# Optimization experiments

Measured on AMD Instinct MI355X. Metric: run time of the kernel, lower is better.

Reference implementation:

```python
import jax, jax.numpy as jnp
import numpy as np

EMBED_DIM = 256
NUM_HEADS = 8
HEAD_DIM = EMBED_DIM // NUM_HEADS
WINDOW = 31
B, S = 4, 2048


def _make_params(key):
    ks = jax.random.split(key, 8)
    sc = 0.05
    Wq = jax.random.normal(ks[0], (NUM_HEADS, EMBED_DIM, HEAD_DIM), jnp.float32) * sc
    bq = jax.random.normal(ks[1], (NUM_HEADS, HEAD_DIM), jnp.float32) * sc
    Wk = jax.random.normal(ks[2], (NUM_HEADS, EMBED_DIM, HEAD_DIM), jnp.float32) * sc
    bk = jax.random.normal(ks[3], (NUM_HEADS, HEAD_DIM), jnp.float32) * sc
    Wv = jax.random.normal(ks[4], (NUM_HEADS, EMBED_DIM, HEAD_DIM), jnp.float32) * sc
    bv = jax.random.normal(ks[5], (NUM_HEADS, HEAD_DIM), jnp.float32) * sc
    Wo = jax.random.normal(ks[6], (NUM_HEADS * HEAD_DIM, EMBED_DIM), jnp.float32) * sc
    bo = jax.random.normal(ks[7], (EMBED_DIM,), jnp.float32) * sc
    return Wq, bq, Wk, bk, Wv, bv, Wo, bo


def setup_inputs() -> dict:
    key = jax.random.key(0)
    k1, k2, k3, k4 = jax.random.split(key, 4)
    eeg = jax.random.normal(k1, (B, S, EMBED_DIM), jnp.float32)
    pps = jax.random.normal(k2, (B, S, EMBED_DIM), jnp.float32)
    e2p = _make_params(k3)
    p2e = _make_params(k4)
    names = ["Wq", "bq", "Wk", "bk", "Wv", "bv", "Wo", "bo"]
    inp = {"eeg": eeg, "pps": pps}
    for n, p in zip(names, e2p):
        inp["e2p_" + n] = p
    for n, p in zip(names, p2e):
        inp["p2e_" + n] = p
    return inp


def _cross_window_attn(q_seq, kv_seq, Wq, bq, Wk, bk, Wv, bv, Wo, bo, window):
    # q_seq, kv_seq: [B, S, D]. Each query position i attends to window of
    # the zero-padded kv sequence centered at i (pad positions get bias-only k/v,
    # matching torch Linear applied to zero vectors).
    b, s, d_in = q_seq.shape
    h, _, hd = Wq.shape
    pad = (window - 1) // 2
    kv_pad = jnp.pad(kv_seq, ((0, 0), (pad, pad), (0, 0)))
    Q = jnp.einsum('bsd,hde->bhse', q_seq, Wq) + bq[None, :, None, :]
    K = jnp.einsum('bsd,hde->bhse', kv_pad, Wk) + bk[None, :, None, :]
    V = jnp.einsum('bsd,hde->bhse', kv_pad, Wv) + bv[None, :, None, :]
    idx = jnp.arange(s)[:, None] + jnp.arange(window)[None, :]  # [S, W]
    Kw = K[:, :, idx, :]  # [B, H, S, W, hd]
    Vw = V[:, :, idx, :]
    scores = jnp.einsum('bhse,bhswe->bhsw', Q, Kw) / np.sqrt(hd).astype(np.float32)
    attn = jax.nn.softmax(scores, axis=-1)
    out = jnp.einsum('bhsw,bhswe->bhse', attn, Vw)  # [B, H, S, hd]
    out = out.transpose(0, 2, 1, 3).reshape(b, s, h * hd)
    return out @ Wo + bo


def reference(eeg, pps,
              e2p_Wq, e2p_bq, e2p_Wk, e2p_bk, e2p_Wv, e2p_bv, e2p_Wo, e2p_bo,
              p2e_Wq, p2e_bq, p2e_Wk, p2e_bk, p2e_Wv, p2e_bv, p2e_Wo, p2e_bo):
    fused_eeg = _cross_window_attn(eeg, pps, e2p_Wq, e2p_bq, e2p_Wk, e2p_bk,
                                   e2p_Wv, e2p_bv, e2p_Wo, e2p_bo, WINDOW)
    fused_pps = _cross_window_attn(pps, eeg, p2e_Wq, p2e_bq, p2e_Wk, p2e_bk,
                                   p2e_Wv, p2e_bv, p2e_Wo, p2e_bo, WINDOW)
    return fused_eeg, fused_pps
```

## Files before the change

kernel.cpp:

```cpp
#include <hip/hip_runtime.h>

static __device__ __forceinline__ float bf2f(unsigned short u) {
    return __uint_as_float(((unsigned int)u) << 16);
}
static __device__ __forceinline__ unsigned short f2bf(float f) {
    unsigned int x = __float_as_uint(f);
    unsigned int lsb = (x >> 16) & 1u;
    x += 0x7fffu + lsb;
    return (unsigned short)(x >> 16);
}

typedef __attribute__((ext_vector_type(8))) short short8;
typedef __attribute__((ext_vector_type(4))) float floatx4;

static __device__ __forceinline__ short8 ldg8(const unsigned short* p) {
    short8 v; __builtin_memcpy(&v, p, 16); return v;
}

__global__ __launch_bounds__(256) void repack_kernel(
    const float* e2p_Wq, const float* e2p_bq,
    const float* e2p_Wk, const float* e2p_bk,
    const float* e2p_Wv, const float* e2p_bv,
    const float* e2p_Wo, const float* e2p_bo,
    const float* p2e_Wq, const float* p2e_bq,
    const float* p2e_Wk, const float* p2e_bk,
    const float* p2e_Wv, const float* p2e_bv,
    const float* p2e_Wo, const float* p2e_bo,
    const float* eeg, const float* pps,
    unsigned short* Wpack, unsigned short* Wopack, float* bias_pack, float* bias2,
    unsigned short* Abf)
{
    int idx = blockIdx.x * 256 + threadIdx.x;
    const int WP = 2 * 768 * 256;
    if (idx < WP) {
        int inp = idx / (768 * 256);
        int rem = idx % (768 * 256);
        int n = rem / 256, k = rem % 256;
        int proj = n / 256, h = (n % 256) / 32, e = n % 32;
        const float* W;
        if (inp == 0) W = (proj == 0) ? e2p_Wq : (proj == 1) ? p2e_Wk : p2e_Wv;
        else          W = (proj == 0) ? p2e_Wq : (proj == 1) ? e2p_Wk : e2p_Wv;
        Wpack[idx] = f2bf(W[h * 8192 + k * 32 + e]);
    }
    int idx2 = idx - WP;
    if (idx2 >= 0 && idx2 < 2 * 65536) {
        int dir = idx2 / 65536, rem2 = idx2 % 65536;
        int n = rem2 / 256, k = rem2 % 256;
        Wopack[idx2] = f2bf((dir == 0 ? e2p_Wo : p2e_Wo)[k * 256 + n]);
    }
    if (idx < 1536) {
        int inp = idx / 768, n = idx % 768;
        int proj = n / 256, he = n % 256;
        const float* bsrc;
        if (inp == 0) bsrc = (proj == 0) ? e2p_bq : (proj == 1) ? p2e_bk : p2e_bv;
        else          bsrc = (proj == 0) ? p2e_bq : (proj == 1) ? e2p_bk : e2p_bv;
        bias_pack[idx] = bsrc[he];
    }
    if (idx >= 1536 && idx < 2048) {
        int j = idx - 1536;
        int dir = j / 256, n = j % 256;
        bias2[j] = (dir == 0 ? e2p_bo : p2e_bo)[n];
    }
    {
        long base = (long)idx * 8;
        const float* src = (base < 2097152) ? eeg : pps;
        long off = (base < 2097152) ? base : base - 2097152;
        float v[8];
        __builtin_memcpy(v, src + off, 32);
        unsigned short o[8];
        #pragma unroll
        for (int j = 0; j < 8; ++j) o[j] = f2bf(v[j]);
        __builtin_memcpy(Abf + base, o, 16);
    }
}

template<bool C_F32>
__global__ __launch_bounds__(256) void mfma_gemm_kernel(
    const unsigned short* __restrict__ A0, const unsigned short* __restrict__ A1,
    const unsigned short* __restrict__ B0t, const unsigned short* __restrict__ B1t,
    const float* __restrict__ bias0, const float* __restrict__ bias1,
    void* __restrict__ C0v, void* __restrict__ C1v,
    int N)
{
    __shared__ __align__(16) unsigned short Cs[128][136];

    const int z = blockIdx.z;
    const unsigned short* A = z ? A1 : A0;
    const unsigned short* Bt = z ? B1t : B0t;
    const float* bias = z ? bias1 : bias0;
    void* Cv = z ? C1v : C0v;

    const int tid = threadIdx.x;
    const long m0 = (long)blockIdx.x * 128;
    const int n0 = blockIdx.y * 128;

    const int lane = tid & 63;
    const int wv = tid >> 6;
    const int wm = (wv >> 1) * 64, wn = (wv & 1) * 64;
    const int fr = lane & 15;
    const int fq = (lane >> 4) * 8;

    const unsigned short* Ap = A + (m0 + wm + fr) * 256 + fq;
    const unsigned short* Bp = Bt + (long)(n0 + wn + fr) * 256 + fq;

    floatx4 acc[4][4] = {};
    short8 af[2][4], bf_[2][4];

    #pragma unroll
    for (int i = 0; i < 4; ++i) af[0][i] = ldg8(Ap + i * 4096);
    #pragma unroll
    for (int j = 0; j < 4; ++j) bf_[0][j] = ldg8(Bp + j * 4096);

    #pragma unroll
    for (int kc = 0; kc < 8; ++kc) {
        const int cur = kc & 1, nxt = cur ^ 1;
        if (kc < 7) {
            const int ko = (kc + 1) * 32;
            #pragma unroll
            for (int i = 0; i < 4; ++i) af[nxt][i] = ldg8(Ap + ko + i * 4096);
            #pragma unroll
            for (int j = 0; j < 4; ++j) bf_[nxt][j] = ldg8(Bp + ko + j * 4096);
        }
        #pragma unroll
        for (int i = 0; i < 4; ++i)
            #pragma unroll
            for (int j = 0; j < 4; ++j)
                acc[i][j] = __builtin_amdgcn_mfma_f32_16x16x32_bf16(af[cur][i], bf_[cur][j], acc[i][j], 0, 0, 0);
    }

    float bj[4];
    #pragma unroll
    for (int j = 0; j < 4; ++j) bj[j] = bias[n0 + wn + j * 16 + fr];

    const int cr0 = wm + ((lane >> 4) << 2);
    #pragma unroll
    for (int i = 0; i < 4; ++i)
        #pragma unroll
        for (int j = 0; j < 4; ++j)
            #pragma unroll
            for (int r = 0; r < 4; ++r)
                Cs[cr0 + i * 16 + r][wn + j * 16 + fr] = f2bf(acc[i][j][r] + bj[j]);
    __syncthreads();

    const int rr = tid >> 4, cc = (tid & 15) * 8;
    #pragma unroll
    for (int p = 0; p < 8; ++p) {
        int r = p * 16 + rr;
        unsigned short tmp[8];
        __builtin_memcpy(tmp, &Cs[r][cc], 16);
        if (C_F32) {
            float of[8];
            #pragma unroll
            for (int j = 0; j < 8; ++j) of[j] = bf2f(tmp[j]);
            __builtin_memcpy((float*)Cv + (m0 + r) * N + n0 + cc, of, 32);
        } else {
            __builtin_memcpy((unsigned short*)Cv + (m0 + r) * N + n0 + cc, tmp, 16);
        }
    }
}

#define KV_STRIDE 138
#define P_STRIDE 72
__global__ __launch_bounds__(256) void attn_kernel(
    const unsigned short* __restrict__ Y, const float* __restrict__ bias_pack,
    unsigned short* __restrict__ att)
{
    __shared__ unsigned short Ks[64][KV_STRIDE];
    __shared__ unsigned short Vs[64][KV_STRIDE];
    __shared__ unsigned short Ps[4][16][P_STRIDE];

    const int s0 = blockIdx.x * 16;
    const int hg = blockIdx.y;
    const int b = blockIdx.z >> 1, dir = blockIdx.z & 1;
    const int kvinp = 1 - dir;
    const int tid = threadIdx.x;

    const float* bkv = bias_pack + kvinp * 768;
    const long kvbase = ((long)kvinp * 8192 + b * 2048) * 768;

    {
        const int r = tid >> 2;
        const int seg = (tid & 3) * 32;
        const int ebase = hg * 128 + seg;
        int p = s0 - 15 + r;
        unsigned short kr[32], vr[32];
        if (p >= 0 && p < 2048) {
            __builtin_memcpy(kr, Y + kvbase + (long)p * 768 + 256 + ebase, 64);
            __builtin_memcpy(vr, Y + kvbase + (long)p * 768 + 512 + ebase, 64);
        } else {
            #pragma unroll
            for (int j = 0; j < 32; ++j) kr[j] = f2bf(bkv[256 + ebase + j]);
            #pragma unroll
            for (int j = 0; j < 32; ++j) vr[j] = f2bf(bkv[512 + ebase + j]);
        }
        __builtin_memcpy(&Ks[r][seg], kr, 64);
        __builtin_memcpy(&Vs[r][seg], vr, 64);
    }

    const int lane = tid & 63;
    const int wv = tid >> 6;
    const int head = hg * 4 + wv;
    const int fr = lane & 15, q4 = lane >> 4;
    short8 aq = ldg8(Y + ((long)dir * 8192 + b * 2048 + s0 + fr) * 768 + head * 32 + q4 * 8);

    __syncthreads();

    floatx4 sacc[4] = {};
    #pragma unroll
    for (int kvt = 0; kvt < 4; ++kvt) {
        short8 bk_ = *(const short8*)&Ks[kvt * 16 + fr][wv * 32 + q4 * 8];
        sacc[kvt] = __builtin_amdgcn_mfma_f32_16x16x32_bf16(aq, bk_, sacc[kvt], 0, 0, 0);
    }

    float sv[4][4];
    float mx[4] = {-3.0e38f, -3.0e38f, -3.0e38f, -3.0e38f};
    #pragma unroll
    for (int kvt = 0; kvt < 4; ++kvt)
        #pragma unroll
        for (int reg = 0; reg < 4; ++reg) {
            int i = q4 * 4 + reg;
            int jc = kvt * 16 + fr;
            int d = jc - i;
            float x = (d >= 0 && d <= 30) ? sacc[kvt][reg] * 0.17677669529663687f : -3.0e38f;
            sv[kvt][reg] = x;
            mx[reg] = fmaxf(mx[reg], x);
        }
    #pragma unroll
    for (int off = 1; off < 16; off <<= 1)
        #pragma unroll
        for (int reg = 0; reg < 4; ++reg)
            mx[reg] = fmaxf(mx[reg], __shfl_xor(mx[reg], off));
    float ps[4] = {};
    #pragma unroll
    for (int kvt = 0; kvt < 4; ++kvt)
        #pragma unroll
        for (int reg = 0; reg < 4; ++reg) {
            float e = __expf(sv[kvt][reg] - mx[reg]);
            sv[kvt][reg] = e;
            ps[reg] += e;
        }
    #pragma unroll
    for (int off = 1; off < 16; off <<= 1)
        #pragma unroll
        for (int reg = 0; reg < 4; ++reg)
            ps[reg] += __shfl_xor(ps[reg], off);

    #pragma unroll
    for (int kvt = 0; kvt < 4; ++kvt)
        #pragma unroll
        for (int reg = 0; reg < 4; ++reg)
            Ps[wv][q4 * 4 + reg][kvt * 16 + fr] = f2bf(sv[kvt][reg]);
    __syncthreads();

    floatx4 oacc[2] = {};
    #pragma unroll
    for (int ch = 0; ch < 2; ++ch) {
        short8 ap = *(const short8*)&Ps[wv][fr][ch * 32 + q4 * 8];
        #pragma unroll
        for (int et = 0; et < 2; ++et) {
            short8 bv;
            #pragma unroll
            for (int j = 0; j < 8; ++j)
                bv[j] = (short)Vs[ch * 32 + q4 * 8 + j][wv * 32 + et * 16 + fr];
            oacc[et] = __builtin_amdgcn_mfma_f32_16x16x32_bf16(ap, bv, oacc[et], 0, 0, 0);
        }
    }

    float rs[4];
    #pragma unroll
    for (int reg = 0; reg < 4; ++reg) rs[reg] = 1.0f / ps[reg];
    #pragma unroll
    for (int et = 0; et < 2; ++et)
        #pragma unroll
        for (int reg = 0; reg < 4; ++reg) {
            int i = q4 * 4 + reg;
            att[((long)dir * 8192 + b * 2048 + s0 + i) * 256 + head * 32 + et * 16 + fr]
                = f2bf(oacc[et][reg] * rs[reg]);
        }
}

extern "C" void kernel_launch(void* const* d_in, const int* in_sizes, int n_in,
                              void* d_out, int out_size, void* d_ws, size_t ws_size,
                              hipStream_t stream)
{
    float* out = (float*)d_out;

    char* ws = (char*)d_ws;
    unsigned short* Wpack   = (unsigned short*)(ws + 0);
    unsigned short* Wopack  = (unsigned short*)(ws + 786432);
    float*          biasP   = (float*)(ws + 1048576);
    float*          bias2   = (float*)(ws + 1054720);
    unsigned short* Y       = (unsigned short*)(ws + 1056768);
    unsigned short* att     = (unsigned short*)(ws + 26222592);
    unsigned short* Abf     = att;

    repack_kernel<<<2048, 256, 0, stream>>>(
        (const float*)d_in[2],  (const float*)d_in[3],
        (const float*)d_in[4],  (const float*)d_in[5],
        (const float*)d_in[6],  (const float*)d_in[7],
        (const float*)d_in[8],  (const float*)d_in[9],
        (const float*)d_in[10], (const float*)d_in[11],
        (const float*)d_in[12], (const float*)d_in[13],
        (const float*)d_in[14], (const float*)d_in[15],
        (const float*)d_in[16], (const float*)d_in[17],
        (const float*)d_in[0],  (const float*)d_in[1],
        Wpack, Wopack, biasP, bias2, Abf);

    mfma_gemm_kernel<false><<<dim3(64, 6, 2), 256, 0, stream>>>(
        Abf, Abf + 2097152, Wpack, Wpack + 196608, biasP, biasP + 768,
        Y, Y + 8192 * 768, 768);

    attn_kernel<<<dim3(128, 2, 8), 256, 0, stream>>>(Y, biasP, att);

    mfma_gemm_kernel<true><<<dim3(64, 2, 2), 256, 0, stream>>>(
        att, att + 2097152, Wopack, Wopack + 65536, bias2, bias2 + 256,
        out, out + 2097152, 256);
}
```

Before: 157.6 us.

## Fuse windowed attention with output projection into one kernel

Merges the attention kernel and the output-projection GEMM into a single kernel. Each block now handles all 8 heads for 16 queries, writes the normalized attention output to shared memory, and multiplies it by Wo read from global memory to produce fp32 output directly. The K tile is trimmed from 64 rows to 48 because only 46 positions are needed; the unused P columns are zero-filled and shared memory is reused across phases. This removes the att round-trip through global memory and one kernel launch. In exchange, each block reloads Wo from global/L2, and the larger 512-thread blocks with more shared memory may lower occupancy.

```diff
diff --git a/kernel.cpp b/kernel.cpp
--- a/kernel.cpp
+++ b/kernel.cpp
@@ -159,19 +159,22 @@
     }
 }
 
-#define KV_STRIDE 138
-#define P_STRIDE 72
-__global__ __launch_bounds__(256) void attn_kernel(
+#define KROWS 48
+#define VROWS 64
+#define KVSTR 264
+__global__ __launch_bounds__(512) void attn_out_kernel(
     const unsigned short* __restrict__ Y, const float* __restrict__ bias_pack,
-    unsigned short* __restrict__ att)
+    const unsigned short* __restrict__ Wopack, const float* __restrict__ bias2,
+    float* __restrict__ out)
 {
-    __shared__ unsigned short Ks[64][KV_STRIDE];
-    __shared__ unsigned short Vs[64][KV_STRIDE];
-    __shared__ unsigned short Ps[4][16][P_STRIDE];
+    __shared__ unsigned short smem[(KROWS + VROWS) * KVSTR];
+    unsigned short* Ks = smem;
+    unsigned short* Vs = smem + KROWS * KVSTR;
+    unsigned short (*Ps)[16][72] = (unsigned short(*)[16][72])smem;
+    unsigned short (*As)[KVSTR] = (unsigned short(*)[KVSTR])smem;
 
     const int s0 = blockIdx.x * 16;
-    const int hg = blockIdx.y;
-    const int b = blockIdx.z >> 1, dir = blockIdx.z & 1;
+    const int b = blockIdx.y, dir = blockIdx.z;
     const int kvinp = 1 - dir;
     const int tid = threadIdx.x;
 
@@ -179,43 +182,46 @@
     const long kvbase = ((long)kvinp * 8192 + b * 2048) * 768;
 
     {
-        const int r = tid >> 2;
-        const int seg = (tid & 3) * 32;
-        const int ebase = hg * 128 + seg;
+        const int r = tid >> 3, seg = (tid & 7) * 32;
         int p = s0 - 15 + r;
-        unsigned short kr[32], vr[32];
+        unsigned short vr[32];
         if (p >= 0 && p < 2048) {
-            __builtin_memcpy(kr, Y + kvbase + (long)p * 768 + 256 + ebase, 64);
-            __builtin_memcpy(vr, Y + kvbase + (long)p * 768 + 512 + ebase, 64);
+            __builtin_memcpy(vr, Y + kvbase + (long)p * 768 + 512 + seg, 64);
         } else {
             #pragma unroll
-            for (int j = 0; j < 32; ++j) kr[j] = f2bf(bkv[256 + ebase + j]);
-            #pragma unroll
-            for (int j = 0; j < 32; ++j) vr[j] = f2bf(bkv[512 + ebase + j]);
-        }
-        __builtin_memcpy(&Ks[r][seg], kr, 64);
-        __builtin_memcpy(&Vs[r][seg], vr, 64);
+            for (int j = 0; j < 32; ++j) vr[j] = f2bf(bkv[512 + seg + j]);
+        }
+        __builtin_memcpy(&Vs[r * KVSTR + seg], vr, 64);
+        if (tid < 384) {
+            unsigned short kr[32];
+            if (p >= 0 && p < 2048) {
+                __builtin_memcpy(kr, Y + kvbase + (long)p * 768 + 256 + seg, 64);
+            } else {
+                #pragma unroll
+                for (int j = 0; j < 32; ++j) kr[j] = f2bf(bkv[256 + seg + j]);
+            }
+            __builtin_memcpy(&Ks[r * KVSTR + seg], kr, 64);
+        }
     }
 
     const int lane = tid & 63;
     const int wv = tid >> 6;
-    const int head = hg * 4 + wv;
     const int fr = lane & 15, q4 = lane >> 4;
-    short8 aq = ldg8(Y + ((long)dir * 8192 + b * 2048 + s0 + fr) * 768 + head * 32 + q4 * 8);
-
-    __syncthreads();
-
-    floatx4 sacc[4] = {};
-    #pragma unroll
-    for (int kvt = 0; kvt < 4; ++kvt) {
-        short8 bk_ = *(const short8*)&Ks[kvt * 16 + fr][wv * 32 + q4 * 8];
+    short8 aq = ldg8(Y + ((long)dir * 8192 + b * 2048 + s0 + fr) * 768 + wv * 32 + q4 * 8);
+
+    __syncthreads();
+
+    floatx4 sacc[3] = {};
+    #pragma unroll
+    for (int kvt = 0; kvt < 3; ++kvt) {
+        short8 bk_ = *(const short8*)&Ks[(kvt * 16 + fr) * KVSTR + wv * 32 + q4 * 8];
         sacc[kvt] = __builtin_amdgcn_mfma_f32_16x16x32_bf16(aq, bk_, sacc[kvt], 0, 0, 0);
     }
 
-    float sv[4][4];
+    float sv[3][4];
     float mx[4] = {-3.0e38f, -3.0e38f, -3.0e38f, -3.0e38f};
     #pragma unroll
-    for (int kvt = 0; kvt < 4; ++kvt)
+    for (int kvt = 0; kvt < 3; ++kvt)
         #pragma unroll
         for (int reg = 0; reg < 4; ++reg) {
             int i = q4 * 4 + reg;
@@ -232,7 +238,7 @@
             mx[reg] = fmaxf(mx[reg], __shfl_xor(mx[reg], off));
     float ps[4] = {};
     #pragma unroll
-    for (int kvt = 0; kvt < 4; ++kvt)
+    for (int kvt = 0; kvt < 3; ++kvt)
         #pragma unroll
         for (int reg = 0; reg < 4; ++reg) {
             float e = __expf(sv[kvt][reg] - mx[reg]);
@@ -245,12 +251,16 @@
         for (int reg = 0; reg < 4; ++reg)
             ps[reg] += __shfl_xor(ps[reg], off);
 
-    #pragma unroll
-    for (int kvt = 0; kvt < 4; ++kvt)
-        #pragma unroll
-        for (int reg = 0; reg < 4; ++reg)
-            Ps[wv][q4 * 4 + reg][kvt * 16 + fr] = f2bf(sv[kvt][reg]);
-    __syncthreads();
+    __syncthreads();
+
+    #pragma unroll
+    for (int reg = 0; reg < 4; ++reg) {
+        int i = q4 * 4 + reg;
+        #pragma unroll
+        for (int kvt = 0; kvt < 3; ++kvt)
+            Ps[wv][i][kvt * 16 + fr] = f2bf(sv[kvt][reg]);
+        Ps[wv][i][48 + fr] = 0;
+    }
 
     floatx4 oacc[2] = {};
     #pragma unroll
@@ -261,7 +271,7 @@
             short8 bv;
             #pragma unroll
             for (int j = 0; j < 8; ++j)
-                bv[j] = (short)Vs[ch * 32 + q4 * 8 + j][wv * 32 + et * 16 + fr];
+                bv[j] = (short)Vs[(ch * 32 + q4 * 8 + j) * KVSTR + wv * 32 + et * 16 + fr];
             oacc[et] = __builtin_amdgcn_mfma_f32_16x16x32_bf16(ap, bv, oacc[et], 0, 0, 0);
         }
     }
@@ -269,13 +279,41 @@
     float rs[4];
     #pragma unroll
     for (int reg = 0; reg < 4; ++reg) rs[reg] = 1.0f / ps[reg];
+
+    __syncthreads();
+
     #pragma unroll
     for (int et = 0; et < 2; ++et)
+        #pragma unroll
+        for (int reg = 0; reg < 4; ++reg)
+            As[q4 * 4 + reg][wv * 32 + et * 16 + fr] = f2bf(oacc[et][reg] * rs[reg]);
+
+    __syncthreads();
+
+    const unsigned short* Wo = Wopack + dir * 65536;
+    const int nw = wv * 32;
+    floatx4 oa[2] = {};
+    #pragma unroll
+    for (int kc = 0; kc < 8; ++kc) {
+        short8 ap = *(const short8*)&As[fr][kc * 32 + q4 * 8];
+        #pragma unroll
+        for (int j = 0; j < 2; ++j) {
+            short8 bw = ldg8(Wo + (nw + j * 16 + fr) * 256 + kc * 32 + q4 * 8);
+            oa[j] = __builtin_amdgcn_mfma_f32_16x16x32_bf16(ap, bw, oa[j], 0, 0, 0);
+        }
+    }
+
+    float bj[2];
+    #pragma unroll
+    for (int j = 0; j < 2; ++j) bj[j] = bias2[dir * 256 + nw + j * 16 + fr];
+
+    float* outp = out + (long)dir * 2097152;
+    #pragma unroll
+    for (int j = 0; j < 2; ++j)
         #pragma unroll
         for (int reg = 0; reg < 4; ++reg) {
             int i = q4 * 4 + reg;
-            att[((long)dir * 8192 + b * 2048 + s0 + i) * 256 + head * 32 + et * 16 + fr]
-                = f2bf(oacc[et][reg] * rs[reg]);
+            outp[((long)b * 2048 + s0 + i) * 256 + nw + j * 16 + fr] = oa[j][reg] + bj[j];
         }
 }
 
@@ -291,8 +329,7 @@
     float*          biasP   = (float*)(ws + 1048576);
     float*          bias2   = (float*)(ws + 1054720);
     unsigned short* Y       = (unsigned short*)(ws + 1056768);
-    unsigned short* att     = (unsigned short*)(ws + 26222592);
-    unsigned short* Abf     = att;
+    unsigned short* Abf     = (unsigned short*)(ws + 26222592);
 
     repack_kernel<<<2048, 256, 0, stream>>>(
         (const float*)d_in[2],  (const float*)d_in[3],
@@ -310,9 +347,5 @@
         Abf, Abf + 2097152, Wpack, Wpack + 196608, biasP, biasP + 768,
         Y, Y + 8192 * 768, 768);
 
-    attn_kernel<<<dim3(128, 2, 8), 256, 0, stream>>>(Y, biasP, att);
-
-    mfma_gemm_kernel<true><<<dim3(64, 2, 2), 256, 0, stream>>>(
-        att, att + 2097152, Wopack, Wopack + 65536, bias2, bias2 + 256,
-        out, out + 2097152, 256);
-}
+    attn_out_kernel<<<dim3(128, 4, 2), 512, 0, stream>>>(Y, biasP, Wopack, bias2, out);
+}
```

Measured after the change: 157.8 us. No clear change (+0.2%).
